# Optimization experiments

Measured on AMD Instinct MI355X. Metric: run time of the kernel, lower is better.

The kernel has to match this reference:

```python
import jax, jax.numpy as jnp
import numpy as np

B, SEQ, DIM = 1, 2048, 4096
N_HEADS, N_KV, HEAD_DIM = 32, 8, 128
N_REP = N_HEADS // N_KV
MAX_CTX = 4096


def setup_inputs() -> dict:
    key = jax.random.key(0)
    ks = jax.random.split(key, 6)
    x = jax.random.normal(ks[0], (B, SEQ, DIM), jnp.float32)
    # RoPE table: (1, SEQ, 1, HEAD_DIM//2, 2) with [cos, sin] in last dim
    inv_freq = 1.0 / (10000.0 ** (jnp.arange(0, HEAD_DIM, 2, dtype=jnp.float32) / HEAD_DIM))
    t = jnp.arange(SEQ, dtype=jnp.float32)
    ang = t[:, None] * inv_freq[None, :]
    freqs_cis = jnp.stack([jnp.cos(ang), jnp.sin(ang)], axis=-1).reshape(1, SEQ, 1, HEAD_DIM // 2, 2)
    cache_kv = jnp.zeros((2, 1, MAX_CTX, N_KV, HEAD_DIM), jnp.float32)
    s = 0.02
    wq = jax.random.normal(ks[1], (DIM, N_HEADS * HEAD_DIM), jnp.float32) * s
    wk = jax.random.normal(ks[2], (DIM, N_KV * HEAD_DIM), jnp.float32) * s
    wv = jax.random.normal(ks[3], (DIM, N_KV * HEAD_DIM), jnp.float32) * s
    wo = jax.random.normal(ks[4], (N_HEADS * HEAD_DIM, DIM), jnp.float32) * s
    return {"x": x, "cache_kv": cache_kv, "freqs_cis": freqs_cis,
            "wq": wq, "wk": wk, "wv": wv, "wo": wo, "start_pos": 0}


def _rope(t, freqs_cis):
    # t: (b, s, h, head_dim); freqs_cis: (1, s, 1, head_dim//2, 2)
    tr = t.reshape(*t.shape[:-1], -1, 2)
    a, b = tr[..., 0], tr[..., 1]
    c, d = freqs_cis[..., 0], freqs_cis[..., 1]
    return jnp.stack([a * c - b * d, a * d + b * c], axis=-1).reshape(t.shape)


def reference(x, cache_kv, freqs_cis, wq, wk, wv, wo, start_pos):
    b, s, _ = x.shape
    xq = (x @ wq).reshape(b, s, N_HEADS, HEAD_DIM)
    xk = (x @ wk).reshape(b, s, N_KV, HEAD_DIM)
    xv = (x @ wv).reshape(b, s, N_KV, HEAD_DIM)
    xq = _rope(xq, freqs_cis)
    xk = _rope(xk, freqs_cis)
    # KV-cache scatter write (start_pos is a static Python int)
    cache = cache_kv.at[:, :, start_pos:start_pos + s].set(jnp.stack([xk, xv]))
    L = start_pos + s
    keys = cache[0, :, :L]    # (b, L, kv, hd)
    values = cache[1, :, :L]
    # GQA without materializing repeats: group q heads by kv head
    q = xq.transpose(0, 2, 1, 3).reshape(b, N_KV, N_REP, s, HEAD_DIM)
    k = keys.transpose(0, 2, 1, 3)     # (b, kv, L, hd)
    v = values.transpose(0, 2, 1, 3)
    scores = jnp.einsum('bkrqd,bkld->bkrql', q, k) * (HEAD_DIM ** -0.5)
    if s > 1:
        mask = jnp.triu(jnp.full((s, L), -jnp.inf, jnp.float32), k=start_pos + 1)
        scores = scores + mask
    p = jax.nn.softmax(scores, axis=-1)
    out = jnp.einsum('bkrql,bkld->bkrqd', p, v)          # (b, kv, rep, s, hd)
    out = out.reshape(b, N_HEADS, s, HEAD_DIM).transpose(0, 2, 1, 3).reshape(b, s, N_HEADS * HEAD_DIM)
    return out @ wo
```

## Files before the change

kernel.cpp:

```cpp
#include <hip/hip_runtime.h>
#include <hip/hip_bf16.h>
#include <stdint.h>

#define SEQ   2048
#define DIM   4096
#define NH    32
#define NKV   8
#define HD    128
#define NREP  4
#define QKVN  6144
#define KOFF  4096
#define VOFF  5120

typedef __bf16 bf16;
typedef __attribute__((ext_vector_type(8))) __bf16 bf16x8;
typedef __attribute__((ext_vector_type(4))) __bf16 bf16x4;
typedef __attribute__((ext_vector_type(4))) float  f32x4;
typedef __attribute__((address_space(1))) void as1_void;
typedef __attribute__((address_space(3))) void as3_void;

__device__ __forceinline__ void async_copy16(void* lds, const void* g) {
  __builtin_amdgcn_global_load_lds((as1_void*)(void*)g, (as3_void*)lds, 16, 0, 0);
}

__device__ __forceinline__ uint32_t pack2bf(float a, float b) {
  union { bf16 h; uint16_t u; } ca, cb;
  ca.h = (bf16)a; cb.h = (bf16)b;
  return (uint32_t)ca.u | ((uint32_t)cb.u << 16);
}

__device__ __forceinline__ void block_barrier() {
  asm volatile("" ::: "memory");
  __builtin_amdgcn_s_barrier();
  asm volatile("" ::: "memory");
}

__global__ __launch_bounds__(256) void cast_x_kernel(const float* __restrict__ src,
                                                     bf16* __restrict__ dst) {
  size_t i = ((size_t)blockIdx.x * 256 + threadIdx.x) * 4;
  const float4 v = *(const float4*)(src + i);
  bf16x4 o;
  o[0] = (bf16)v.x; o[1] = (bf16)v.y; o[2] = (bf16)v.z; o[3] = (bf16)v.w;
  *(bf16x4*)(dst + i) = o;
}

__global__ __launch_bounds__(256) void transpose_cast_kernel(const float* __restrict__ src,
                                                             bf16* __restrict__ dst,
                                                             int R, int C) {
  __shared__ float tile[64][65];
  const int c0 = blockIdx.x * 64, r0 = blockIdx.y * 64;
  const int tx = threadIdx.x & 15, ty = threadIdx.x >> 4;
#pragma unroll
  for (int p = 0; p < 4; ++p) {
    float4 v = *(const float4*)&src[(size_t)(r0 + ty + p*16) * C + c0 + tx*4];
    tile[ty + p*16][tx*4+0] = v.x;
    tile[ty + p*16][tx*4+1] = v.y;
    tile[ty + p*16][tx*4+2] = v.z;
    tile[ty + p*16][tx*4+3] = v.w;
  }
  __syncthreads();
  const int k = threadIdx.x & 15;
  const int g = threadIdx.x >> 4;
#pragma unroll
  for (int p = 0; p < 4; ++p) {
    int X = g + 16*p;
    bf16x4 o;
    o[0] = (bf16)tile[4*k+0][X];
    o[1] = (bf16)tile[4*k+1][X];
    o[2] = (bf16)tile[4*k+2][X];
    o[3] = (bf16)tile[4*k+3][X];
    *(bf16x4*)&dst[(size_t)(c0 + X) * R + r0 + 4*k] = o;
  }
}

template<int OUT_F32, int ROPE>
__global__ __launch_bounds__(512, 2) void gemm256_kernel(const bf16* __restrict__ A,
                                                         const bf16* __restrict__ Bt,
                                                         void* __restrict__ Cout,
                                                         int M, int N, int K,
                                                         const float* __restrict__ fr) {
  __shared__ __align__(16) bf16 As[32768];
  __shared__ __align__(16) bf16 Bs[32768];
  char* AsB = (char*)As;
  char* BsB = (char*)Bs;

  const int tid  = threadIdx.x;
  const int w    = tid >> 6, lane = tid & 63;
  const int lane16 = lane & 15, quad = lane >> 4;
  const int wm = w >> 2, wn = w & 3;

  const int nwg = gridDim.x * gridDim.y;
  int bid = blockIdx.y * gridDim.x + blockIdx.x;
  bid = (bid & 7) * (nwg >> 3) + (bid >> 3);
  const int bx = bid % gridDim.x, by = bid / gridDim.x;
  const int bm = by * 256, bn = bx * 256;

  const int NT = K >> 6;

  const int qsw = ((quad ^ (lane16 & 3)) << 4);
  const uint32_t aLane = (uint32_t)(wm*128 + lane16) * 64 + qsw;
  const uint32_t bLane = (uint32_t)(wn*64  + lane16) * 64 + qsw;

  auto stageA = [&](int buf, int t, int ks) {
#pragma unroll
    for (int i = 0; i < 2; ++i) {
      int c = tid + (i << 9);
      int row = c >> 2;
      int q = ((c & 3) ^ (row & 3)) << 3;
      async_copy16(AsB + buf*32768 + ks*16384 + c*16,
                   A + (size_t)(bm + row) * K + t*64 + ks*32 + q);
    }
  };
  auto stageB = [&](int buf, int t, int ks) {
#pragma unroll
    for (int i = 0; i < 2; ++i) {
      int c = tid + (i << 9);
      int row = c >> 2;
      int q = ((c & 3) ^ (row & 3)) << 3;
      async_copy16(BsB + buf*32768 + ks*16384 + c*16,
                   Bt + (size_t)(bn + row) * K + t*64 + ks*32 + q);
    }
  };

  f32x4 acc[8][4] = {};

#define LD_A(DST, BUF, KS, QM)                                                        \
  do {                                                                                \
    _Pragma("unroll")                                                                 \
    for (int ii = 0; ii < 4; ++ii)                                                    \
      (DST)[ii] = *(const bf16x8*)(AsB + (BUF)*32768 + (KS)*16384 + aLane             \
                                   + ((QM)*4 + ii) * 1024);                           \
  } while (0)
#define LD_B(DST, BUF, KS)                                                            \
  do {                                                                                \
    _Pragma("unroll")                                                                 \
    for (int jj = 0; jj < 4; ++jj)                                                    \
      (DST)[jj] = *(const bf16x8*)(BsB + (BUF)*32768 + (KS)*16384 + bLane             \
                                   + jj * 1024);                                      \
  } while (0)
#define MMA_PHASE(AF, BF, QM)                                                         \
  do {                                                                                \
    __builtin_amdgcn_s_setprio(1);                                                    \
    _Pragma("unroll")                                                                 \
    for (int jj = 0; jj < 4; ++jj)                                                    \
      _Pragma("unroll")                                                               \
      for (int ii = 0; ii < 4; ++ii)                                                  \
        acc[(QM)*4 + ii][jj] = __builtin_amdgcn_mfma_f32_16x16x32_bf16(               \
            (AF)[ii], (BF)[jj], acc[(QM)*4 + ii][jj], 0, 0, 0);                       \
    __builtin_amdgcn_s_setprio(0);                                                    \
  } while (0)

  stageA(0, 0, 0); stageB(0, 0, 0); stageA(0, 0, 1); stageB(0, 0, 1);
  stageA(1, 1, 0); stageB(1, 1, 0);
  asm volatile("s_waitcnt vmcnt(4)" ::: "memory");
  block_barrier();

  for (int t = 0; t < NT; ++t) {
    const int cb = t & 1, nb = cb ^ 1;
    bf16x8 af[4], bf0[4], bf1[4];

    LD_A(af, cb, 0, 0);
    LD_B(bf0, cb, 0);
    if (t + 1 < NT) stageA(nb, t + 1, 1);
    block_barrier();
    MMA_PHASE(af, bf0, 0);
    block_barrier();

    LD_A(af, cb, 0, 1);
    if (t + 1 < NT) stageB(nb, t + 1, 1);
    block_barrier();
    MMA_PHASE(af, bf0, 1);
    block_barrier();

    LD_A(af, cb, 1, 0);
    LD_B(bf1, cb, 1);
    if (t + 2 < NT) stageA(cb, t + 2, 0);
    block_barrier();
    MMA_PHASE(af, bf1, 0);
    block_barrier();

    LD_A(af, cb, 1, 1);
    if (t + 2 < NT) stageB(cb, t + 2, 0);
    block_barrier();
    MMA_PHASE(af, bf1, 1);
    if (t + 2 < NT) asm volatile("s_waitcnt vmcnt(4)" ::: "memory");
    else            asm volatile("s_waitcnt vmcnt(0)" ::: "memory");
    block_barrier();
  }

#pragma unroll
  for (int i = 0; i < 8; ++i)
#pragma unroll
    for (int j = 0; j < 4; ++j) {
      const int colb = bn + wn*64 + j*16;
      const bool do_rope = ROPE && colb < 5120;
      const int p2 = (colb + lane16) & 126;
#pragma unroll
      for (int r = 0; r < 4; ++r) {
        size_t row = (size_t)bm + wm*128 + i*16 + quad*4 + r;
        size_t col = (size_t)colb + lane16;
        float v = acc[i][j][r];
        if (ROPE) {
          float vp = __shfl_xor(v, 1);
          if (do_rope) {
            float2 cd = *(const float2*)&fr[row*128 + p2];
            v = (lane16 & 1) ? (vp*cd.y + v*cd.x) : (v*cd.x - vp*cd.y);
          }
        }
        if (OUT_F32) ((float*)Cout)[row * N + col] = v;
        else         ((bf16*)Cout)[row * N + col] = (bf16)v;
      }
    }
#undef LD_A
#undef LD_B
#undef MMA_PHASE
}

__global__ __launch_bounds__(256) void transpose_v_kernel(const bf16* __restrict__ qkv,
                                                          bf16* __restrict__ vt) {
  __shared__ bf16 tile[32][33];
  int tt = blockIdx.x * 32;
  int dd = blockIdx.y * 32;
  int kv = blockIdx.z;
  int tx = threadIdx.x & 31, ty = threadIdx.x >> 5;
  const bf16* src = qkv + VOFF + kv * HD;
#pragma unroll
  for (int j = 0; j < 4; ++j)
    tile[ty + j*8][tx] = src[(size_t)(tt + ty + j*8) * QKVN + dd + tx];
  __syncthreads();
  bf16* dst = vt + ((size_t)kv * HD + dd) * SEQ + tt;
#pragma unroll
  for (int j = 0; j < 4; ++j)
    dst[(size_t)(ty + j*8) * SEQ + tx] = tile[tx][ty + j*8];
}

__global__ __launch_bounds__(256, 3) void flash_attn_kernel(const bf16* __restrict__ qkv,
                                                            const bf16* __restrict__ vt,
                                                            bf16* __restrict__ out) {
  __shared__ __align__(16) bf16 Ks[4*96*32];
  __shared__ __align__(16) bf16 Vts[3*128*32];
  const int b  = blockIdx.x;
  const int qt = 31 - (b >> 5);
  const int h  = b & 31;
  const int kvh = h >> 2;
  const int tid = threadIdx.x;
  const int w = tid >> 6, lane = tid & 63;
  const int lane16 = lane & 15, quad = lane >> 4;
  const float scale = 0.08838834764831845f;
  const int qglob = qt*64 + w*16 + lane16;

  const bf16* qrow = qkv + (size_t)qglob * QKVN + h * HD + quad*8;
  bf16x8 qreg[4];
#pragma unroll
  for (int kk = 0; kk < 4; ++kk)
    qreg[kk] = *(const bf16x8*)(qrow + kk*32);

  f32x4 acc_o[8] = {};
  float m_s = -3e38f, l_s = 0.f;

  const bf16* kbase0 = qkv + KOFF + kvh * HD;
  const bf16* vbase0 = vt + (size_t)kvh * HD * SEQ;

  const int L = (qt*64 + 159) / 96;
  for (int jj = 0; jj < L; ++jj) {
    const int kv0 = jj * 96;
    __syncthreads();
#pragma unroll
    for (int i = 0; i < 6; ++i) {
      int c = tid + i * 256;
      {
        int kk = c / 384, rem = c - kk*384;
        async_copy16(&Ks[c*8], kbase0 + (size_t)(kv0 + (rem >> 2)) * QKVN + kk*32 + (rem & 3) * 8);
      }
      {
        int kk2 = c >> 9, cp = c & 511;
        async_copy16(&Vts[c*8], vbase0 + (size_t)(cp >> 2) * SEQ + kv0 + kk2*32 + (cp & 3) * 8);
      }
    }
    __syncthreads();

    f32x4 accT[6] = {};
#pragma unroll
    for (int kk = 0; kk < 4; ++kk)
#pragma unroll
      for (int jn = 0; jn < 6; ++jn) {
        bf16x8 kf = *(const bf16x8*)&Ks[(kk*96 + jn*16 + lane16)*32 + quad*8];
        accT[jn] = __builtin_amdgcn_mfma_f32_16x16x32_bf16(kf, qreg[kk], accT[jn], 0, 0, 0);
      }

    float s[6][4];
#pragma unroll
    for (int jn = 0; jn < 6; ++jn)
#pragma unroll
      for (int r = 0; r < 4; ++r) {
        float v = accT[jn][r] * scale;
        if ((kv0 + jn*16 + quad*4 + r) > qglob) v = -3e38f;
        s[jn][r] = v;
      }

    float mt = s[0][0];
#pragma unroll
    for (int jn = 0; jn < 6; ++jn)
#pragma unroll
      for (int r = 0; r < 4; ++r) mt = fmaxf(mt, s[jn][r]);
    mt = fmaxf(mt, __shfl_xor(mt, 16));
    mt = fmaxf(mt, __shfl_xor(mt, 32));
    float mnew = fmaxf(m_s, mt);
    float alpha = __expf(m_s - mnew);
    m_s = mnew;
    float rs = 0.f;
#pragma unroll
    for (int jn = 0; jn < 6; ++jn)
#pragma unroll
      for (int r = 0; r < 4; ++r) {
        float p = __expf(s[jn][r] - mnew);
        s[jn][r] = p;
        rs += p;
      }
    rs += __shfl_xor(rs, 16);
    rs += __shfl_xor(rs, 32);
    l_s = l_s * alpha + rs;

    float alpha_row[4];
#pragma unroll
    for (int r = 0; r < 4; ++r)
      alpha_row[r] = __shfl(alpha, quad*4 + r);
#pragma unroll
    for (int jd = 0; jd < 8; ++jd)
#pragma unroll
      for (int r = 0; r < 4; ++r) acc_o[jd][r] *= alpha_row[r];

    uint32_t pk[6][2];
#pragma unroll
    for (int jn = 0; jn < 6; ++jn) {
      pk[jn][0] = pack2bf(s[jn][0], s[jn][1]);
      pk[jn][1] = pack2bf(s[jn][2], s[jn][3]);
    }

    const int src0 = (quad & 1) * 32 + lane16;
    const int src1 = src0 + 16;
    const bool hi = quad >= 2;
#pragma unroll
    for (int kk2 = 0; kk2 < 3; ++kk2) {
      uint32_t v0l = __shfl(pk[2*kk2][0],   src0), v0h = __shfl(pk[2*kk2][1],   src0);
      uint32_t v1l = __shfl(pk[2*kk2][0],   src1), v1h = __shfl(pk[2*kk2][1],   src1);
      uint32_t w0l = __shfl(pk[2*kk2+1][0], src0), w0h = __shfl(pk[2*kk2+1][1], src0);
      uint32_t w1l = __shfl(pk[2*kk2+1][0], src1), w1h = __shfl(pk[2*kk2+1][1], src1);
      union { uint32_t u[4]; bf16x8 v; } af;
      af.u[0] = hi ? w0l : v0l;
      af.u[1] = hi ? w0h : v0h;
      af.u[2] = hi ? w1l : v1l;
      af.u[3] = hi ? w1h : v1h;
#pragma unroll
      for (int jd = 0; jd < 8; ++jd) {
        bf16x8 vf = *(const bf16x8*)&Vts[(kk2*128 + jd*16 + lane16)*32 + quad*8];
        acc_o[jd] = __builtin_amdgcn_mfma_f32_16x16x32_bf16(af.v, vf, acc_o[jd], 0, 0, 0);
      }
    }
  }

  const float inv_l = 1.f / l_s;
  float linv[4];
#pragma unroll
  for (int r = 0; r < 4; ++r)
    linv[r] = __shfl(inv_l, quad*4 + r);

  bf16* obase = out + (size_t)(qt*64 + w*16) * DIM + h * HD;
#pragma unroll
  for (int jd = 0; jd < 8; ++jd)
#pragma unroll
    for (int r = 0; r < 4; ++r)
      obase[(size_t)(quad*4 + r) * DIM + jd*16 + lane16] = (bf16)(acc_o[jd][r] * linv[r]);
}

extern "C" void kernel_launch(void* const* d_in, const int* in_sizes, int n_in,
                              void* d_out, int out_size, void* d_ws, size_t ws_size,
                              hipStream_t stream) {
  const float* x  = (const float*)d_in[0];
  const float* fr = (const float*)d_in[2];
  const float* wq = (const float*)d_in[3];
  const float* wk = (const float*)d_in[4];
  const float* wv = (const float*)d_in[5];
  const float* wo = (const float*)d_in[6];
  float* out = (float*)d_out;

  char* ws = (char*)d_ws;
  bf16* xb     = (bf16*)(ws);
  bf16* wqkv_t = (bf16*)(ws + 16777216);
  bf16* wo_t   = (bf16*)(ws + 67108864);
  bf16* qkv    = (bf16*)(ws + 100663296);
  bf16* vt     = (bf16*)(ws + 125829120);
  bf16* attn   = (bf16*)(ws + 130023424);
  (void)ws_size; (void)in_sizes; (void)n_in; (void)out_size;

  cast_x_kernel<<<8192, 256, 0, stream>>>(x, xb);
  transpose_cast_kernel<<<dim3(64,64), 256, 0, stream>>>(wq, wqkv_t, DIM, DIM);
  transpose_cast_kernel<<<dim3(16,64), 256, 0, stream>>>(wk, wqkv_t + (size_t)4096*4096, DIM, 1024);
  transpose_cast_kernel<<<dim3(16,64), 256, 0, stream>>>(wv, wqkv_t + (size_t)5120*4096, DIM, 1024);
  transpose_cast_kernel<<<dim3(64,64), 256, 0, stream>>>(wo, wo_t, DIM, DIM);

  gemm256_kernel<0,1><<<dim3(24,8), 512, 0, stream>>>(xb, wqkv_t, qkv, SEQ, QKVN, DIM, fr);
  transpose_v_kernel<<<dim3(64,4,8), 256, 0, stream>>>(qkv, vt);
  flash_attn_kernel<<<1024, 256, 0, stream>>>(qkv, vt, attn);
  gemm256_kernel<1,0><<<dim3(16,8), 512, 0, stream>>>(attn, wo_t, out, SEQ, DIM, DIM, nullptr);
}
```

Before: 625.6 us.

## Parameterize GEMM N-tile width and rework LDS layout for more workgroups

Templates the GEMM on the N tile width, using 192 for the QKV projection and 128 for the output projection, so each GEMM launches 256 workgroups instead of 192 or 128. This fills the device's 256 compute units better. The LDS layout changes from XOR-swizzled rows to a k-chunk-major layout, and B is staged once per k-tile rather than in two halves. Explicit lgkmcnt waits and sched barriers are added before the MFMA phases, and the vmcnt thresholds are retuned to match. The trade-off is less data reuse per tile, possible LDS bank conflicts from the unswizzled layout, and a more serialized schedule.

```diff
diff --git a/kernel.cpp b/kernel.cpp
--- a/kernel.cpp
+++ b/kernel.cpp
@@ -73,16 +73,16 @@
   }
 }
 
-template<int OUT_F32, int ROPE>
+template<int OUT_F32, int ROPE, int BN>
 __global__ __launch_bounds__(512, 2) void gemm256_kernel(const bf16* __restrict__ A,
                                                          const bf16* __restrict__ Bt,
                                                          void* __restrict__ Cout,
                                                          int M, int N, int K,
                                                          const float* __restrict__ fr) {
-  __shared__ __align__(16) bf16 As[32768];
-  __shared__ __align__(16) bf16 Bs[32768];
-  char* AsB = (char*)As;
-  char* BsB = (char*)Bs;
+  constexpr int BNF = BN / 64;
+  constexpr int BCH = BN / 64;
+  constexpr int BBYTES = BN * 128;
+  __shared__ __align__(16) char lds[65536 + 2 * BBYTES];
 
   const int tid  = threadIdx.x;
   const int w    = tid >> 6, lane = tid & 63;
@@ -93,71 +93,73 @@
   int bid = blockIdx.y * gridDim.x + blockIdx.x;
   bid = (bid & 7) * (nwg >> 3) + (bid >> 3);
   const int bx = bid % gridDim.x, by = bid / gridDim.x;
-  const int bm = by * 256, bn = bx * 256;
+  const int bm = by * 256, bn = bx * BN;
 
   const int NT = K >> 6;
-
-  const int qsw = ((quad ^ (lane16 & 3)) << 4);
-  const uint32_t aLane = (uint32_t)(wm*128 + lane16) * 64 + qsw;
-  const uint32_t bLane = (uint32_t)(wn*64  + lane16) * 64 + qsw;
 
   auto stageA = [&](int buf, int t, int ks) {
 #pragma unroll
     for (int i = 0; i < 2; ++i) {
       int c = tid + (i << 9);
-      int row = c >> 2;
-      int q = ((c & 3) ^ (row & 3)) << 3;
-      async_copy16(AsB + buf*32768 + ks*16384 + c*16,
-                   A + (size_t)(bm + row) * K + t*64 + ks*32 + q);
+      int q = c >> 8, row = c & 255;
+      async_copy16(lds + buf*32768 + ks*16384 + c*16,
+                   A + (size_t)(bm + row) * K + t*64 + ks*32 + q*8);
     }
   };
-  auto stageB = [&](int buf, int t, int ks) {
-#pragma unroll
-    for (int i = 0; i < 2; ++i) {
+  auto stageB = [&](int buf, int t) {
+#pragma unroll
+    for (int i = 0; i < BCH; ++i) {
       int c = tid + (i << 9);
-      int row = c >> 2;
-      int q = ((c & 3) ^ (row & 3)) << 3;
-      async_copy16(BsB + buf*32768 + ks*16384 + c*16,
-                   Bt + (size_t)(bn + row) * K + t*64 + ks*32 + q);
+      int ks = c / (BN*4), r = c - ks*(BN*4);
+      int q = r / BN, col = r - q*BN;
+      async_copy16(lds + 65536 + buf*BBYTES + c*16,
+                   Bt + (size_t)(bn + col) * K + t*64 + ks*32 + q*8);
     }
   };
 
-  f32x4 acc[8][4] = {};
+  f32x4 acc[8][BNF] = {};
 
 #define LD_A(DST, BUF, KS, QM)                                                        \
   do {                                                                                \
     _Pragma("unroll")                                                                 \
     for (int ii = 0; ii < 4; ++ii)                                                    \
-      (DST)[ii] = *(const bf16x8*)(AsB + (BUF)*32768 + (KS)*16384 + aLane             \
-                                   + ((QM)*4 + ii) * 1024);                           \
+      (DST)[ii] = *(const bf16x8*)(lds + (BUF)*32768 + (KS)*16384 +                   \
+          (quad*256 + wm*128 + (QM)*64 + ii*16 + lane16) * 16);                       \
   } while (0)
 #define LD_B(DST, BUF, KS)                                                            \
   do {                                                                                \
     _Pragma("unroll")                                                                 \
-    for (int jj = 0; jj < 4; ++jj)                                                    \
-      (DST)[jj] = *(const bf16x8*)(BsB + (BUF)*32768 + (KS)*16384 + bLane             \
-                                   + jj * 1024);                                      \
+    for (int jj = 0; jj < BNF; ++jj)                                                  \
+      (DST)[jj] = *(const bf16x8*)(lds + 65536 + (BUF)*BBYTES +                       \
+          (((KS)*4 + quad)*BN + wn*(BN/4) + jj*16 + lane16) * 16);                    \
   } while (0)
 #define MMA_PHASE(AF, BF, QM)                                                         \
   do {                                                                                \
+    asm volatile("s_waitcnt lgkmcnt(0)" ::: "memory");                                \
+    __builtin_amdgcn_sched_barrier(0);                                                \
     __builtin_amdgcn_s_setprio(1);                                                    \
     _Pragma("unroll")                                                                 \
-    for (int jj = 0; jj < 4; ++jj)                                                    \
+    for (int jj = 0; jj < BNF; ++jj)                                                  \
       _Pragma("unroll")                                                               \
       for (int ii = 0; ii < 4; ++ii)                                                  \
         acc[(QM)*4 + ii][jj] = __builtin_amdgcn_mfma_f32_16x16x32_bf16(               \
             (AF)[ii], (BF)[jj], acc[(QM)*4 + ii][jj], 0, 0, 0);                       \
     __builtin_amdgcn_s_setprio(0);                                                    \
   } while (0)
-
-  stageA(0, 0, 0); stageB(0, 0, 0); stageA(0, 0, 1); stageB(0, 0, 1);
-  stageA(1, 1, 0); stageB(1, 1, 0);
-  asm volatile("s_waitcnt vmcnt(4)" ::: "memory");
+#define VM_WAIT_STEADY()                                                              \
+  do {                                                                                \
+    if constexpr (BN == 192) asm volatile("s_waitcnt vmcnt(7)" ::: "memory");         \
+    else                     asm volatile("s_waitcnt vmcnt(6)" ::: "memory");         \
+  } while (0)
+
+  stageA(0, 0, 0); stageB(0, 0); stageA(0, 0, 1);
+  stageA(1, 1, 0); stageB(1, 1);
+  VM_WAIT_STEADY();
   block_barrier();
 
   for (int t = 0; t < NT; ++t) {
     const int cb = t & 1, nb = cb ^ 1;
-    bf16x8 af[4], bf0[4], bf1[4];
+    bf16x8 af[4], bf0[BNF], bf1[BNF];
 
     LD_A(af, cb, 0, 0);
     LD_B(bf0, cb, 0);
@@ -167,9 +169,10 @@
     block_barrier();
 
     LD_A(af, cb, 0, 1);
-    if (t + 1 < NT) stageB(nb, t + 1, 1);
     block_barrier();
     MMA_PHASE(af, bf0, 1);
+    if (t + 1 < NT) VM_WAIT_STEADY();
+    else            asm volatile("s_waitcnt vmcnt(0)" ::: "memory");
     block_barrier();
 
     LD_A(af, cb, 1, 0);
@@ -180,19 +183,20 @@
     block_barrier();
 
     LD_A(af, cb, 1, 1);
-    if (t + 2 < NT) stageB(cb, t + 2, 0);
+    if (t + 2 < NT) stageB(cb, t + 2);
     block_barrier();
     MMA_PHASE(af, bf1, 1);
-    if (t + 2 < NT) asm volatile("s_waitcnt vmcnt(4)" ::: "memory");
-    else            asm volatile("s_waitcnt vmcnt(0)" ::: "memory");
+    if (t + 2 < NT)      VM_WAIT_STEADY();
+    else if (t + 1 < NT) asm volatile("s_waitcnt vmcnt(2)" ::: "memory");
+    else                 asm volatile("s_waitcnt vmcnt(0)" ::: "memory");
     block_barrier();
   }
 
 #pragma unroll
   for (int i = 0; i < 8; ++i)
 #pragma unroll
-    for (int j = 0; j < 4; ++j) {
-      const int colb = bn + wn*64 + j*16;
+    for (int j = 0; j < BNF; ++j) {
+      const int colb = bn + wn*(BN/4) + j*16;
       const bool do_rope = ROPE && colb < 5120;
       const int p2 = (colb + lane16) & 126;
 #pragma unroll
@@ -214,6 +218,7 @@
 #undef LD_A
 #undef LD_B
 #undef MMA_PHASE
+#undef VM_WAIT_STEADY
 }
 
 __global__ __launch_bounds__(256) void transpose_v_kernel(const bf16* __restrict__ qkv,
@@ -399,8 +404,8 @@
   transpose_cast_kernel<<<dim3(16,64), 256, 0, stream>>>(wv, wqkv_t + (size_t)5120*4096, DIM, 1024);
   transpose_cast_kernel<<<dim3(64,64), 256, 0, stream>>>(wo, wo_t, DIM, DIM);
 
-  gemm256_kernel<0,1><<<dim3(24,8), 512, 0, stream>>>(xb, wqkv_t, qkv, SEQ, QKVN, DIM, fr);
+  gemm256_kernel<0,1,192><<<dim3(32,8), 512, 0, stream>>>(xb, wqkv_t, qkv, SEQ, QKVN, DIM, fr);
   transpose_v_kernel<<<dim3(64,4,8), 256, 0, stream>>>(qkv, vt);
   flash_attn_kernel<<<1024, 256, 0, stream>>>(qkv, vt, attn);
-  gemm256_kernel<1,0><<<dim3(16,8), 512, 0, stream>>>(attn, wo_t, out, SEQ, DIM, DIM, nullptr);
-}
+  gemm256_kernel<1,0,128><<<dim3(32,8), 512, 0, stream>>>(attn, wo_t, out, SEQ, DIM, DIM, nullptr);
+}
```

New measurement: 621.1 us. No clear change (-0.7%).
